# Optimization experiments

Hardware: AMD Instinct MI355X
Metric: run time of the kernel (lower is better)

The kernel has to match this reference:

```python
import jax, jax.numpy as jnp
import numpy as np
from jax import lax

MAX_COC = 50.0
NUM_PLANES = 32
B, C, H, W = 4, 3, 512, 512


def _gaussian_kernel_np(coc_value):
    # static (trace-time) kernel construction, mirroring the torch code
    sigma = coc_value / 2.355
    k = int(2 * coc_value + 1)
    if k % 2 == 0:
        k += 1
    k = min(k, 31)
    coords = np.arange(k, dtype=np.float32) - (k // 2)
    g = np.exp(-coords ** 2 / (2.0 * sigma ** 2))
    g = g / g.sum()
    return np.outer(g, g).astype(np.float32)  # [k, k]


def _depthwise_blur(x, kern2d):
    # depthwise (groups=C) 2D conv with 'same' padding, NCHW layout
    c = x.shape[1]
    k = kern2d.shape[0]
    w = jnp.broadcast_to(jnp.asarray(kern2d, x.dtype)[None, None], (c, 1, k, k))
    pad = k // 2
    return lax.conv_general_dilated(
        x, w, window_strides=(1, 1), padding=[(pad, pad), (pad, pad)],
        dimension_numbers=('NCHW', 'OIHW', 'NCHW'), feature_group_count=c)


def setup_inputs() -> dict:
    key = jax.random.key(0)
    k1, k2 = jax.random.split(key)
    sharp_image = jax.random.uniform(k1, (B, C, H, W), dtype=jnp.float32)
    # CoC values spanning [0, MAX_COC] so all depth-plane buckets are hit
    coc_map = jax.random.uniform(k2, (B, 1, H, W), dtype=jnp.float32) * MAX_COC
    return {"sharp_image": sharp_image, "coc_map": coc_map}


def reference(sharp_image, coc_map):
    planes = np.linspace(0.0, MAX_COC, NUM_PLANES, dtype=np.float32)
    result = jnp.zeros_like(sharp_image)
    for i in range(NUM_PLANES):  # fixed small loop over depth planes
        coc = float(planes[i])
        if coc < 0.5:
            blurred = sharp_image
        else:
            blurred = _depthwise_blur(sharp_image, _gaussian_kernel_np(coc))
        if i == 0:
            wgt = (coc_map <= (planes[0] + planes[1]) / 2).astype(sharp_image.dtype)
        elif i == NUM_PLANES - 1:
            wgt = (coc_map > (planes[-2] + planes[-1]) / 2).astype(sharp_image.dtype)
        else:
            lower = (planes[i - 1] + planes[i]) / 2
            upper = (planes[i] + planes[i + 1]) / 2
            wgt = ((coc_map > lower) & (coc_map <= upper)).astype(sharp_image.dtype)
        # accumulate instead of stacking: same math as (stack * weights).sum(0)
        result = result + blurred * wgt
    return result
```

## Files before the change

### kernel.cpp

```cpp
#include <hip/hip_runtime.h>

typedef _Float16 f16;
typedef _Float16 f16x2 __attribute__((ext_vector_type(2)));
typedef _Float16 f16x4 __attribute__((ext_vector_type(4)));
typedef _Float16 f16x8 __attribute__((ext_vector_type(8)));
typedef float    f32x4 __attribute__((ext_vector_type(4)));

#define KW 31
#define R  15
#define NP 32
#define HH 512
#define WW 512
#define NB 4

#define TW 32
#define TH 32
#define EXT_X 62
#define SX 80
#define EXT_Y 63
#define GH_S 81
#define GY_S 36

__global__ __launch_bounds__(256, 1) void defocus_kernel(
    const float* __restrict__ sharp, const float* __restrict__ coc_map,
    float* __restrict__ out)
{
    __shared__ __align__(16) f16 tile[3][EXT_Y][SX];
    __shared__ __align__(16) f16 gTh[NP][GH_S];
    __shared__ __align__(16) f16 gTy[NP][GY_S];
    __shared__ unsigned char pl8[TH][TW];
    __shared__ float bnd[KW];

    const int tid = threadIdx.x;
    const int bx = blockIdx.x, by = blockIdx.y, bb = blockIdx.z;

    if (tid < NP) {
        const int p = tid;
        for (int i = 0; i < GH_S; ++i) gTh[p][i] = (f16)0.0f;
        for (int i = 0; i < GY_S; ++i) gTy[p][i] = (f16)0.0f;
        const double step = 50.0 / 31.0;
        const float pv = (p == 31) ? 50.0f : (float)((double)p * step);
        if (pv < 0.5f) {
            gTh[p][15 + R] = (f16)1.0f;
            gTy[p][R]      = (f16)1.0f;
        } else {
            const double coc   = (double)pv;
            const double sigma = coc / 2.355;
            int k = (int)(2.0 * coc + 1.0);
            if ((k & 1) == 0) k += 1;
            if (k > KW) k = KW;
            const int half = k >> 1;
            float s = 0.0f;
            for (int j = 0; j < k; ++j) {
                double c = (double)(j - half);
                s += (float)exp(-(c * c) / (2.0 * sigma * sigma));
            }
            for (int j = 0; j < k; ++j) {
                double c = (double)(j - half);
                const float w = (float)exp(-(c * c) / (2.0 * sigma * sigma)) / s;
                const int d = R - half + j;
                gTh[p][15 + d] = (f16)w;
                gTy[p][d]      = (f16)w;
            }
        }
    }
    if (tid < KW) {
        const double step = 50.0 / 31.0;
        const float pa = (float)((double)tid * step);
        const float pb = (tid == 30) ? 50.0f : (float)((double)(tid + 1) * step);
        bnd[tid] = (pa + pb) * 0.5f;
    }
    __syncthreads();

    {
        const int row = tid >> 3;
        const int x4  = (tid & 7) * 4;
        const float4 c4 = *(const float4*)&coc_map[((size_t)bb * HH + by * TH + row) * WW + bx * TW + x4];
        const float cv[4] = {c4.x, c4.y, c4.z, c4.w};
        int pp[4] = {0, 0, 0, 0};
        #pragma unroll
        for (int k = 0; k < KW; ++k) {
            const float b = bnd[k];
            pp[0] += (cv[0] > b) ? 1 : 0;
            pp[1] += (cv[1] > b) ? 1 : 0;
            pp[2] += (cv[2] > b) ? 1 : 0;
            pp[3] += (cv[3] > b) ? 1 : 0;
        }
        *(uchar4*)&pl8[row][x4] = make_uchar4((unsigned char)pp[0], (unsigned char)pp[1],
                                              (unsigned char)pp[2], (unsigned char)pp[3]);
    }

    for (int idx = tid; idx < 3 * EXT_Y * (SX / 2); idx += 256) {
        const int dw = idx % (SX / 2);
        const int rr = (idx / (SX / 2)) % EXT_Y;
        const int ch = idx / ((SX / 2) * EXT_Y);
        const int gy  = by * TH - R + rr;
        const int gxa = bx * TW - R + 2 * dw;
        float va = 0.0f, vb = 0.0f;
        if (rr < 62 && (unsigned)gy < HH) {
            const float* src = &sharp[(((size_t)bb * 3 + ch) * HH + gy) * WW];
            if (2 * dw     < EXT_X && (unsigned)gxa       < WW) va = src[gxa];
            if (2 * dw + 1 < EXT_X && (unsigned)(gxa + 1) < WW) vb = src[gxa + 1];
        }
        f16x2 h; h.x = (f16)va; h.y = (f16)vb;
        *(f16x2*)&tile[ch][rr][2 * dw] = h;
    }
    __syncthreads();

    const int lid = tid & 63, wv = tid >> 6;
    const int c = lid & 15, q = lid >> 4;

    #pragma unroll 2
    for (int t = wv; t < 64; t += 4) {
        const int sx = t >> 5, r = t & 31;
        const int xs = sx * 16;

        const int pm = pl8[r][xs + c];
        f16x8 b0, b1;
        #pragma unroll
        for (int j = 0; j < 8; ++j) {
            b0[j] = gTh[pm][q * 8 + j      - c + 15];
            b1[j] = gTh[pm][q * 8 + j + 32 - c + 15];
        }

        const f16x4 wyA = *(const f16x4*)&gTy[pm][4 * q];
        const f16x4 wyB = *(const f16x4*)&gTy[pm][16 + 4 * q];

        float o[3];
        #pragma unroll
        for (int ch = 0; ch < 3; ++ch) {
            float s = 0.0f;
            #pragma unroll
            for (int nt = 0; nt < 2; ++nt) {
                const f16* ap = &tile[ch][r + nt * 16 + c][xs + q * 8];
                const f16x8 a0 = *(const f16x8*)ap;
                const f16x8 a1 = *(const f16x8*)(ap + 32);
                f32x4 acc = {0.f, 0.f, 0.f, 0.f};
                acc = __builtin_amdgcn_mfma_f32_16x16x32_f16(a0, b0, acc, 0, 0, 0);
                acc = __builtin_amdgcn_mfma_f32_16x16x32_f16(a1, b1, acc, 0, 0, 0);
                const f16x4 wy = nt ? wyB : wyA;
                #pragma unroll
                for (int i = 0; i < 4; ++i) s = fmaf((float)wy[i], acc[i], s);
            }
            o[ch] = s;
        }

        #pragma unroll
        for (int ch = 0; ch < 3; ++ch) {
            o[ch] += __shfl_xor(o[ch], 16, 64);
            o[ch] += __shfl_xor(o[ch], 32, 64);
        }

        if (q == 0) {
            const int ox = bx * TW + xs + c;
            const int oy = by * TH + r;
            #pragma unroll
            for (int ch = 0; ch < 3; ++ch)
                out[(((size_t)bb * 3 + ch) * HH + oy) * WW + ox] = o[ch];
        }
    }
}

extern "C" void kernel_launch(void* const* d_in, const int* in_sizes, int n_in,
                              void* d_out, int out_size, void* d_ws, size_t ws_size,
                              hipStream_t stream) {
    const float* sharp = (const float*)d_in[0];
    const float* coc   = (const float*)d_in[1];
    float* outp        = (float*)d_out;
    dim3 grid(WW / TW, HH / TH, NB);
    defocus_kernel<<<grid, dim3(256), 0, stream>>>(sharp, coc, outp);
}
```

Baseline: 119.6 us.

## Switch per-pixel blur MFMA from 16x16x32 to 32x32x16 tiles

Replaces the two-slice 16x16x32 MFMA scheme with 32x32x16 MFMAs covering a full 32-pixel row per wave. The per-plane kernel table becomes two copies, one shifted by a single element, so B fragments load as aligned f16x2 pairs instead of scalar gathers. The reduction needs one cross-lane shuffle instead of two. The aim is fewer fragment-build instructions and shuffles per output. The trade-off is more MFMA work and accumulator registers per row, and a smaller padded tile stride that may change LDS bank conflicts.

```diff
diff --git a/kernel.cpp b/kernel.cpp
--- a/kernel.cpp
+++ b/kernel.cpp
@@ -4,7 +4,7 @@
 typedef _Float16 f16x2 __attribute__((ext_vector_type(2)));
 typedef _Float16 f16x4 __attribute__((ext_vector_type(4)));
 typedef _Float16 f16x8 __attribute__((ext_vector_type(8)));
-typedef float    f32x4 __attribute__((ext_vector_type(4)));
+typedef float    f32x16 __attribute__((ext_vector_type(16)));
 
 #define KW 31
 #define R  15
@@ -16,18 +16,17 @@
 #define TW 32
 #define TH 32
 #define EXT_X 62
-#define SX 80
+#define SX 72
 #define EXT_Y 63
-#define GH_S 81
-#define GY_S 36
+#define GB 32
+#define GT_S 98
 
 __global__ __launch_bounds__(256, 1) void defocus_kernel(
     const float* __restrict__ sharp, const float* __restrict__ coc_map,
     float* __restrict__ out)
 {
     __shared__ __align__(16) f16 tile[3][EXT_Y][SX];
-    __shared__ __align__(16) f16 gTh[NP][GH_S];
-    __shared__ __align__(16) f16 gTy[NP][GY_S];
+    __shared__ __align__(16) f16 gTh2[NP][2][GT_S];
     __shared__ unsigned char pl8[TH][TW];
     __shared__ float bnd[KW];
 
@@ -36,13 +35,11 @@
 
     if (tid < NP) {
         const int p = tid;
-        for (int i = 0; i < GH_S; ++i) gTh[p][i] = (f16)0.0f;
-        for (int i = 0; i < GY_S; ++i) gTy[p][i] = (f16)0.0f;
+        for (int i = 0; i < GT_S; ++i) gTh2[p][0][i] = (f16)0.0f;
         const double step = 50.0 / 31.0;
         const float pv = (p == 31) ? 50.0f : (float)((double)p * step);
         if (pv < 0.5f) {
-            gTh[p][15 + R] = (f16)1.0f;
-            gTy[p][R]      = (f16)1.0f;
+            gTh2[p][0][GB + R] = (f16)1.0f;
         } else {
             const double coc   = (double)pv;
             const double sigma = coc / 2.355;
@@ -58,11 +55,11 @@
             for (int j = 0; j < k; ++j) {
                 double c = (double)(j - half);
                 const float w = (float)exp(-(c * c) / (2.0 * sigma * sigma)) / s;
-                const int d = R - half + j;
-                gTh[p][15 + d] = (f16)w;
-                gTy[p][d]      = (f16)w;
+                gTh2[p][0][GB + (R - half + j)] = (f16)w;
             }
         }
+        for (int i = 0; i < GT_S - 1; ++i) gTh2[p][1][i] = gTh2[p][0][i + 1];
+        gTh2[p][1][GT_S - 1] = (f16)0.0f;
     }
     if (tid < KW) {
         const double step = 50.0 / 31.0;
@@ -108,52 +105,55 @@
     __syncthreads();
 
     const int lid = tid & 63, wv = tid >> 6;
-    const int c = lid & 15, q = lid >> 4;
+    const int c32 = lid & 31, h = lid >> 5;
+    const int cp = c32 & 1;
+    const int dwb0 = (GB + 8 * h - c32) >> 1;
+
+    union U8 { f16x2 h2[4]; f16x8 h8; };
 
     #pragma unroll 2
-    for (int t = wv; t < 64; t += 4) {
-        const int sx = t >> 5, r = t & 31;
-        const int xs = sx * 16;
+    for (int r = wv; r < TH; r += 4) {
+        const int pm = pl8[r][c32];
+        const f16* tab = &gTh2[pm][cp][0];
 
-        const int pm = pl8[r][xs + c];
-        f16x8 b0, b1;
+        U8 bf[4];
         #pragma unroll
-        for (int j = 0; j < 8; ++j) {
-            b0[j] = gTh[pm][q * 8 + j      - c + 15];
-            b1[j] = gTh[pm][q * 8 + j + 32 - c + 15];
-        }
+        for (int kc = 0; kc < 4; ++kc)
+            #pragma unroll
+            for (int n = 0; n < 4; ++n)
+                bf[kc].h2[n] = *(const f16x2*)&tab[2 * (dwb0 + 8 * kc + n)];
 
-        const f16x4 wyA = *(const f16x4*)&gTy[pm][4 * q];
-        const f16x4 wyB = *(const f16x4*)&gTy[pm][16 + 4 * q];
+        f16x4 wy[4];
+        #pragma unroll
+        for (int a = 0; a < 4; ++a)
+            wy[a] = *(const f16x4*)&gTh2[pm][0][GB + 8 * a + 4 * h];
 
         float o[3];
         #pragma unroll
         for (int ch = 0; ch < 3; ++ch) {
+            const f16* ap = &tile[ch][r + c32][8 * h];
+            f32x16 acc;
+            #pragma unroll
+            for (int i = 0; i < 16; ++i) acc[i] = 0.0f;
+            acc = __builtin_amdgcn_mfma_f32_32x32x16_f16(*(const f16x8*)(ap     ), bf[0].h8, acc, 0, 0, 0);
+            acc = __builtin_amdgcn_mfma_f32_32x32x16_f16(*(const f16x8*)(ap + 16), bf[1].h8, acc, 0, 0, 0);
+            acc = __builtin_amdgcn_mfma_f32_32x32x16_f16(*(const f16x8*)(ap + 32), bf[2].h8, acc, 0, 0, 0);
+            acc = __builtin_amdgcn_mfma_f32_32x32x16_f16(*(const f16x8*)(ap + 48), bf[3].h8, acc, 0, 0, 0);
             float s = 0.0f;
             #pragma unroll
-            for (int nt = 0; nt < 2; ++nt) {
-                const f16* ap = &tile[ch][r + nt * 16 + c][xs + q * 8];
-                const f16x8 a0 = *(const f16x8*)ap;
-                const f16x8 a1 = *(const f16x8*)(ap + 32);
-                f32x4 acc = {0.f, 0.f, 0.f, 0.f};
-                acc = __builtin_amdgcn_mfma_f32_16x16x32_f16(a0, b0, acc, 0, 0, 0);
-                acc = __builtin_amdgcn_mfma_f32_16x16x32_f16(a1, b1, acc, 0, 0, 0);
-                const f16x4 wy = nt ? wyB : wyA;
+            for (int a = 0; a < 4; ++a)
                 #pragma unroll
-                for (int i = 0; i < 4; ++i) s = fmaf((float)wy[i], acc[i], s);
-            }
+                for (int b = 0; b < 4; ++b)
+                    s = fmaf((float)wy[a][b], acc[4 * a + b], s);
             o[ch] = s;
         }
 
         #pragma unroll
-        for (int ch = 0; ch < 3; ++ch) {
-            o[ch] += __shfl_xor(o[ch], 16, 64);
-            o[ch] += __shfl_xor(o[ch], 32, 64);
-        }
+        for (int ch = 0; ch < 3; ++ch) o[ch] += __shfl_xor(o[ch], 32, 64);
 
-        if (q == 0) {
-            const int ox = bx * TW + xs + c;
+        if (h == 0) {
             const int oy = by * TH + r;
+            const int ox = bx * TW + c32;
             #pragma unroll
             for (int ch = 0; ch < 3; ++ch)
                 out[(((size_t)bb * 3 + ch) * HH + oy) * WW + ox] = o[ch];
```

New measurement: 105.4 us. 1.14x faster.
